# Optimization experiments

Measured on AMD Instinct MI355X. Metric: run time of the kernel, lower is better.

## Reference

```python
import jax, jax.numpy as jnp
import numpy as np
from jax import lax

BATCH = 8192
HID = 10
IN = 64
STEPS = 512
REVERSE = True


def setup_inputs() -> dict:
    key = jax.random.key(0)
    ks = jax.random.split(key, 9)
    s_in = 1.0 / np.sqrt(HID)
    return {
        "hidden": jax.random.normal(ks[0], (1, BATCH, HID), dtype=jnp.float32),
        "w_ih": jax.random.uniform(ks[1], (3 * HID, IN), jnp.float32, -s_in, s_in),
        "w_hh": jax.random.uniform(ks[2], (3 * HID, HID), jnp.float32, -s_in, s_in),
        "b_ih": jax.random.uniform(ks[3], (3 * HID,), jnp.float32, -s_in, s_in),
        "b_hh": jax.random.uniform(ks[4], (3 * HID,), jnp.float32, -s_in, s_in),
        "l1_w": jax.random.uniform(ks[5], (10, HID), jnp.float32, -s_in, s_in),
        "l1_b": jax.random.uniform(ks[6], (10,), jnp.float32, -s_in, s_in),
        "l2_w": jax.random.uniform(ks[7], (IN, 10), jnp.float32, -s_in, s_in),
        "l2_b": jax.random.uniform(ks[8], (IN,), jnp.float32, -s_in, s_in),
        "step": STEPS,
    }


def _gru_cell(h, x, w_ih, w_hh, b_ih, b_hh):
    # PyTorch GRU gate order: reset, update, new
    gi = x @ w_ih.T + b_ih  # [B, 3H]
    gh = h @ w_hh.T + b_hh  # [B, 3H]
    i_r, i_z, i_n = jnp.split(gi, 3, axis=-1)
    h_r, h_z, h_n = jnp.split(gh, 3, axis=-1)
    r = jax.nn.sigmoid(i_r + h_r)
    z = jax.nn.sigmoid(i_z + h_z)
    n = jnp.tanh(i_n + r * h_n)
    return (1.0 - z) * n + z * h


def reference(hidden, w_ih, w_hh, b_ih, b_hh, l1_w, l1_b, l2_w, l2_b, step):
    h0 = hidden[0]  # [B, H]
    B = h0.shape[0]
    x0 = jnp.zeros((B, IN), dtype=h0.dtype)  # first GRU input is zeros

    def body(carry, _):
        h, x = carry
        h_new = _gru_cell(h, x, w_ih, w_hh, b_ih, b_hh)
        o = h_new @ l1_w.T + l1_b          # l1 on GRU output
        x_next = o @ l2_w.T + l2_b         # l2 feeds next GRU step
        return (h_new, x_next), o

    _, outs = lax.scan(body, (h0, x0), None, length=step)  # [T, B, 10]
    outs = jnp.transpose(outs, (1, 0, 2))  # [B, T, 10]
    if REVERSE:
        outs = outs[:, ::-1, :]
    return outs
```

## Files before the change

kernel.cpp:

```cpp
#include <hip/hip_runtime.h>

#define HID 10
#define STEPS 512

typedef __attribute__((ext_vector_type(2))) float v2f;

template<int F>
static __device__ __forceinline__ float swz(float v) {
    return __int_as_float(__builtin_amdgcn_ds_swizzle(__float_as_int(v), (F << 5) | 0x10));
}

__global__ __launch_bounds__(64, 2) void gru_decoder_kernel(
    const float* __restrict__ hidden, const float* __restrict__ w_ih,
    const float* __restrict__ w_hh, const float* __restrict__ b_ih,
    const float* __restrict__ b_hh, const float* __restrict__ l1_w,
    const float* __restrict__ l1_b, const float* __restrict__ l2_w,
    const float* __restrict__ l2_b, float* __restrict__ out)
{
    __shared__ float sWx[640];
    __shared__ float sbx[64];
    __shared__ float sWgi[300];
    __shared__ float sbgi[30];
    __shared__ float sWhh[300];

    const int lane = threadIdx.x;
    const int f    = lane & 15;
    const int b    = blockIdx.x * 4 + (lane >> 4);
    const bool ok  = (f < HID);
    const int fi   = ok ? f : 0;

    for (int e = lane; e < 640; e += 64) {
        int i = e / 10, j = e - i * 10;
        float acc = 0.f;
        #pragma unroll
        for (int k = 0; k < 10; ++k) acc += l2_w[i * 10 + k] * l1_w[k * 10 + j];
        sWx[e] = acc;
    }
    {
        float acc = l2_b[lane];
        #pragma unroll
        for (int k = 0; k < 10; ++k) acc += l2_w[lane * 10 + k] * l1_b[k];
        sbx[lane] = acc;
    }
    for (int e = lane; e < 300; e += 64) sWhh[e] = w_hh[e];
    __syncthreads();
    for (int e = lane; e < 300; e += 64) {
        int m = e / 10, j = e - m * 10;
        float acc = 0.f;
        for (int k = 0; k < 64; ++k) acc += w_ih[m * 64 + k] * sWx[k * 10 + j];
        sWgi[e] = acc;
    }
    if (lane < 30) {
        float acc = b_ih[lane];
        for (int k = 0; k < 64; ++k) acc += w_ih[lane * 64 + k] * sbx[k];
        sbgi[lane] = acc;
    }
    __syncthreads();

    const float LOG2E = 1.4426950408889634f;
    const float S2    = 2.f * LOG2E;

    v2f wrz[10], wnn[10];
    float wo[10];
    #pragma unroll
    for (int k = 0; k < 10; ++k) {
        float grz_r = -(sWgi[fi * 10 + k] + sWhh[fi * 10 + k]) * LOG2E;
        float grz_z = -(sWgi[(10 + fi) * 10 + k] + sWhh[(10 + fi) * 10 + k]) * LOG2E;
        float gni   = sWgi[(20 + fi) * 10 + k] * S2;
        float gnh   = sWhh[(20 + fi) * 10 + k] * S2;
        wrz[k] = ok ? v2f{grz_r, grz_z} : v2f{0.f, 0.f};
        wnn[k] = ok ? v2f{gni, gnh} : v2f{0.f, 0.f};
        wo[k]  = ok ? l1_w[fi * 10 + k] : 0.f;
    }
    const v2f brz = ok ? v2f{-(sbgi[fi] + b_hh[fi]) * LOG2E,
                             -(sbgi[10 + fi] + b_hh[10 + fi]) * LOG2E}
                       : v2f{0.f, 0.f};
    const v2f bnn = ok ? v2f{sbgi[20 + fi] * S2, b_hh[20 + fi] * S2} : v2f{0.f, 0.f};
    const float bo = ok ? l1_b[fi] : 0.f;
    const v2f brz0 = ok ? v2f{-(b_ih[fi] + b_hh[fi]) * LOG2E,
                              -(b_ih[10 + fi] + b_hh[10 + fi]) * LOG2E}
                        : v2f{0.f, 0.f};
    const float bni0 = ok ? b_ih[20 + fi] * S2 : 0.f;

    float h = ok ? hidden[(size_t)b * HID + f] : 0.f;

    float ha[10];
    #define GATHER()                                                       \
        ha[0] = swz<0>(h); ha[1] = swz<1>(h); ha[2] = swz<2>(h);           \
        ha[3] = swz<3>(h); ha[4] = swz<4>(h); ha[5] = swz<5>(h);           \
        ha[6] = swz<6>(h); ha[7] = swz<7>(h); ha[8] = swz<8>(h);           \
        ha[9] = swz<9>(h);

    GATHER();

    float* pb = out + (size_t)b * (STEPS * HID) + (size_t)(STEPS - 1) * HID + f;

    #define O_AND_STORE()                                                  \
        {                                                                  \
            float o = bo;                                                  \
            _Pragma("unroll")                                              \
            for (int k = 0; k < 10; ++k) o += wo[k] * ha[k];               \
            if (ok) pb[0] = o;                                             \
            pb -= HID;                                                     \
        }

    {
        float pr = 0.f, pz = 0.f, ph = 0.f;
        #pragma unroll
        for (int k = 0; k < 10; ++k) {
            pr += sWhh[fi * 10 + k] * ha[k];
            pz += sWhh[(10 + fi) * 10 + k] * ha[k];
            ph += sWhh[(20 + fi) * 10 + k] * ha[k];
        }
        float vr = brz0.x - pr * LOG2E;
        float vz = brz0.y - pz * LOG2E;
        float r = __builtin_amdgcn_rcpf(1.f + __builtin_amdgcn_exp2f(vr));
        float z = __builtin_amdgcn_rcpf(1.f + __builtin_amdgcn_exp2f(vz));
        float y = bni0 + r * (ph * S2 + bnn.y);
        float n = 1.f - 2.f * __builtin_amdgcn_rcpf(1.f + __builtin_amdgcn_exp2f(y));
        h = ok ? (n + z * (h - n)) : 0.f;
        GATHER();
        O_AND_STORE();
    }

    #pragma unroll 1
    for (int t = 1; t < STEPS; ++t) {
        v2f arz = brz, ann = bnn;
        #pragma unroll
        for (int k = 0; k < 10; ++k) {
            v2f hh = {ha[k], ha[k]};
            arz += wrz[k] * hh;
            ann += wnn[k] * hh;
        }
        float r = __builtin_amdgcn_rcpf(1.f + __builtin_amdgcn_exp2f(arz.x));
        float z = __builtin_amdgcn_rcpf(1.f + __builtin_amdgcn_exp2f(arz.y));
        float y = ann.x + r * ann.y;
        float n = 1.f - 2.f * __builtin_amdgcn_rcpf(1.f + __builtin_amdgcn_exp2f(y));
        h = n + z * (h - n);
        GATHER();
        O_AND_STORE();
    }
}

extern "C" void kernel_launch(void* const* d_in, const int* in_sizes, int n_in,
                              void* d_out, int out_size, void* d_ws, size_t ws_size,
                              hipStream_t stream) {
    (void)in_sizes; (void)n_in; (void)d_ws; (void)ws_size; (void)out_size;
    dim3 grid(2048), block(64);
    gru_decoder_kernel<<<grid, block, 0, stream>>>(
        (const float*)d_in[0], (const float*)d_in[1], (const float*)d_in[2],
        (const float*)d_in[3], (const float*)d_in[4], (const float*)d_in[5],
        (const float*)d_in[6], (const float*)d_in[7], (const float*)d_in[8],
        (float*)d_out);
}
```

Baseline: 317.1 us.

## Replace ds_swizzle broadcasts with DPP row rotations and fuse output dot into gate loop

Replaces the ten ds_swizzle broadcasts per step with fifteen DPP row_ror rotations of h, and permutes each lane's weights so they line up with the rotated source indices. The output projection is computed from the same rotated h values inside the gate loop, with the store lagging one step and a final epilogue writing the last output. The accumulation is split into two independent chains to shorten the dependency chain. DPP moves avoid the LDS-path latency of swizzle, but the step now does 16 multiply-adds per gate instead of 10, with zero padding.

```diff
diff --git a/kernel.cpp b/kernel.cpp
--- a/kernel.cpp
+++ b/kernel.cpp
@@ -8,6 +8,16 @@
 template<int F>
 static __device__ __forceinline__ float swz(float v) {
     return __int_as_float(__builtin_amdgcn_ds_swizzle(__float_as_int(v), (F << 5) | 0x10));
+}
+
+template<int J>
+static __device__ __forceinline__ float frot(float v) {
+    return __int_as_float(__builtin_amdgcn_update_dpp(
+        0, __float_as_int(v), 0x120 + J, 0xF, 0xF, true));
+}
+template<int J>
+static __device__ __forceinline__ int irot(int v) {
+    return __builtin_amdgcn_update_dpp(0, v, 0x120 + J, 0xF, 0xF, true);
 }
 
 __global__ __launch_bounds__(64, 2) void gru_decoder_kernel(
@@ -60,18 +70,30 @@
     const float LOG2E = 1.4426950408889634f;
     const float S2    = 2.f * LOG2E;
 
-    v2f wrz[10], wnn[10];
-    float wo[10];
+    int sidx[16];
+    sidx[0]  = f;
+    sidx[1]  = irot<1>(f);   sidx[2]  = irot<2>(f);   sidx[3]  = irot<3>(f);
+    sidx[4]  = irot<4>(f);   sidx[5]  = irot<5>(f);   sidx[6]  = irot<6>(f);
+    sidx[7]  = irot<7>(f);   sidx[8]  = irot<8>(f);   sidx[9]  = irot<9>(f);
+    sidx[10] = irot<10>(f);  sidx[11] = irot<11>(f);  sidx[12] = irot<12>(f);
+    sidx[13] = irot<13>(f);  sidx[14] = irot<14>(f);  sidx[15] = irot<15>(f);
+
+    v2f wrz[16], wnn[16];
+    float wo[16];
     #pragma unroll
-    for (int k = 0; k < 10; ++k) {
-        float grz_r = -(sWgi[fi * 10 + k] + sWhh[fi * 10 + k]) * LOG2E;
-        float grz_z = -(sWgi[(10 + fi) * 10 + k] + sWhh[(10 + fi) * 10 + k]) * LOG2E;
-        float gni   = sWgi[(20 + fi) * 10 + k] * S2;
-        float gnh   = sWhh[(20 + fi) * 10 + k] * S2;
-        wrz[k] = ok ? v2f{grz_r, grz_z} : v2f{0.f, 0.f};
-        wnn[k] = ok ? v2f{gni, gnh} : v2f{0.f, 0.f};
-        wo[k]  = ok ? l1_w[fi * 10 + k] : 0.f;
-    }
+    for (int j = 0; j < 16; ++j) {
+        int s   = sidx[j];
+        bool va = ok && (s < HID);
+        int sc  = (s < HID) ? s : 0;
+        float grz_r = -(sWgi[fi * 10 + sc] + sWhh[fi * 10 + sc]) * LOG2E;
+        float grz_z = -(sWgi[(10 + fi) * 10 + sc] + sWhh[(10 + fi) * 10 + sc]) * LOG2E;
+        float gni   = sWgi[(20 + fi) * 10 + sc] * S2;
+        float gnh   = sWhh[(20 + fi) * 10 + sc] * S2;
+        wrz[j] = va ? v2f{grz_r, grz_z} : v2f{0.f, 0.f};
+        wnn[j] = va ? v2f{gni, gnh}     : v2f{0.f, 0.f};
+        wo[j]  = va ? l1_w[fi * 10 + sc] : 0.f;
+    }
+
     const v2f brz = ok ? v2f{-(sbgi[fi] + b_hh[fi]) * LOG2E,
                              -(sbgi[10 + fi] + b_hh[10 + fi]) * LOG2E}
                        : v2f{0.f, 0.f};
@@ -84,27 +106,14 @@
 
     float h = ok ? hidden[(size_t)b * HID + f] : 0.f;
 
-    float ha[10];
-    #define GATHER()                                                       \
-        ha[0] = swz<0>(h); ha[1] = swz<1>(h); ha[2] = swz<2>(h);           \
-        ha[3] = swz<3>(h); ha[4] = swz<4>(h); ha[5] = swz<5>(h);           \
-        ha[6] = swz<6>(h); ha[7] = swz<7>(h); ha[8] = swz<8>(h);           \
+    float* pb = out + (size_t)b * (STEPS * HID) + (size_t)(STEPS - 1) * HID + f;
+
+    {
+        float ha[10];
+        ha[0] = swz<0>(h); ha[1] = swz<1>(h); ha[2] = swz<2>(h);
+        ha[3] = swz<3>(h); ha[4] = swz<4>(h); ha[5] = swz<5>(h);
+        ha[6] = swz<6>(h); ha[7] = swz<7>(h); ha[8] = swz<8>(h);
         ha[9] = swz<9>(h);
-
-    GATHER();
-
-    float* pb = out + (size_t)b * (STEPS * HID) + (size_t)(STEPS - 1) * HID + f;
-
-    #define O_AND_STORE()                                                  \
-        {                                                                  \
-            float o = bo;                                                  \
-            _Pragma("unroll")                                              \
-            for (int k = 0; k < 10; ++k) o += wo[k] * ha[k];               \
-            if (ok) pb[0] = o;                                             \
-            pb -= HID;                                                     \
-        }
-
-    {
         float pr = 0.f, pz = 0.f, ph = 0.f;
         #pragma unroll
         for (int k = 0; k < 10; ++k) {
@@ -119,26 +128,65 @@
         float y = bni0 + r * (ph * S2 + bnn.y);
         float n = 1.f - 2.f * __builtin_amdgcn_rcpf(1.f + __builtin_amdgcn_exp2f(y));
         h = ok ? (n + z * (h - n)) : 0.f;
-        GATHER();
-        O_AND_STORE();
     }
 
     #pragma unroll 1
     for (int t = 1; t < STEPS; ++t) {
-        v2f arz = brz, ann = bnn;
-        #pragma unroll
-        for (int k = 0; k < 10; ++k) {
-            v2f hh = {ha[k], ha[k]};
-            arz += wrz[k] * hh;
-            ann += wnn[k] * hh;
+        float rh[16];
+        rh[0]  = h;
+        rh[1]  = frot<1>(h);   rh[2]  = frot<2>(h);   rh[3]  = frot<3>(h);
+        rh[4]  = frot<4>(h);   rh[5]  = frot<5>(h);   rh[6]  = frot<6>(h);
+        rh[7]  = frot<7>(h);   rh[8]  = frot<8>(h);   rh[9]  = frot<9>(h);
+        rh[10] = frot<10>(h);  rh[11] = frot<11>(h);  rh[12] = frot<12>(h);
+        rh[13] = frot<13>(h);  rh[14] = frot<14>(h);  rh[15] = frot<15>(h);
+
+        v2f a0 = brz, n0 = bnn;
+        v2f a1 = {0.f, 0.f}, n1 = {0.f, 0.f};
+        float o0 = bo, o1 = 0.f;
+        #pragma unroll
+        for (int j = 0; j < 8; ++j) {
+            v2f hj = {rh[j], rh[j]};
+            a0 += wrz[j] * hj;
+            n0 += wnn[j] * hj;
+            o0 = __builtin_fmaf(wo[j], rh[j], o0);
         }
+        #pragma unroll
+        for (int j = 8; j < 16; ++j) {
+            v2f hj = {rh[j], rh[j]};
+            a1 += wrz[j] * hj;
+            n1 += wnn[j] * hj;
+            o1 = __builtin_fmaf(wo[j], rh[j], o1);
+        }
+        v2f arz = a0 + a1;
+        v2f ann = n0 + n1;
+        float o = o0 + o1;
+
         float r = __builtin_amdgcn_rcpf(1.f + __builtin_amdgcn_exp2f(arz.x));
         float z = __builtin_amdgcn_rcpf(1.f + __builtin_amdgcn_exp2f(arz.y));
-        float y = ann.x + r * ann.y;
+        float zh  = z * h;
+        float omz = 1.f - z;
+        float y = __builtin_fmaf(r, ann.y, ann.x);
         float n = 1.f - 2.f * __builtin_amdgcn_rcpf(1.f + __builtin_amdgcn_exp2f(y));
-        h = n + z * (h - n);
-        GATHER();
-        O_AND_STORE();
+        h = __builtin_fmaf(n, omz, zh);
+
+        if (ok) pb[0] = o;
+        pb -= HID;
+    }
+
+    {
+        float rh[16];
+        rh[0]  = h;
+        rh[1]  = frot<1>(h);   rh[2]  = frot<2>(h);   rh[3]  = frot<3>(h);
+        rh[4]  = frot<4>(h);   rh[5]  = frot<5>(h);   rh[6]  = frot<6>(h);
+        rh[7]  = frot<7>(h);   rh[8]  = frot<8>(h);   rh[9]  = frot<9>(h);
+        rh[10] = frot<10>(h);  rh[11] = frot<11>(h);  rh[12] = frot<12>(h);
+        rh[13] = frot<13>(h);  rh[14] = frot<14>(h);  rh[15] = frot<15>(h);
+        float o0 = bo, o1 = 0.f;
+        #pragma unroll
+        for (int j = 0; j < 8; ++j)  o0 = __builtin_fmaf(wo[j], rh[j], o0);
+        #pragma unroll
+        for (int j = 8; j < 16; ++j) o1 = __builtin_fmaf(wo[j], rh[j], o1);
+        if (ok) pb[0] = o0 + o1;
     }
 }
 
```

Measured after the change: 348.5 us. +9.9%, slower.

## Fuse output projection into next step's packed matvec over h-pairs

Applied to the files above, without the earlier changes.

Repacks the weights so that packed float2 FMAs run along the reduction dimension, covering pairs of hidden elements. The output projection is folded into the same loop as the gate matvecs of the next step, with a final epilogue for the last output. This removes the separate 10-FMA output dot product from the critical path and reorders the h update so z*h can start before n is known. In exchange it adds horizontal-sum adds and a different floating-point summation order.

```diff
diff --git a/kernel.cpp b/kernel.cpp
--- a/kernel.cpp
+++ b/kernel.cpp
@@ -60,51 +60,45 @@
     const float LOG2E = 1.4426950408889634f;
     const float S2    = 2.f * LOG2E;
 
-    v2f wrz[10], wnn[10];
-    float wo[10];
+    v2f wr2[5], wz2[5], wi2[5], wh2[5], wo2[5];
     #pragma unroll
-    for (int k = 0; k < 10; ++k) {
-        float grz_r = -(sWgi[fi * 10 + k] + sWhh[fi * 10 + k]) * LOG2E;
-        float grz_z = -(sWgi[(10 + fi) * 10 + k] + sWhh[(10 + fi) * 10 + k]) * LOG2E;
-        float gni   = sWgi[(20 + fi) * 10 + k] * S2;
-        float gnh   = sWhh[(20 + fi) * 10 + k] * S2;
-        wrz[k] = ok ? v2f{grz_r, grz_z} : v2f{0.f, 0.f};
-        wnn[k] = ok ? v2f{gni, gnh} : v2f{0.f, 0.f};
-        wo[k]  = ok ? l1_w[fi * 10 + k] : 0.f;
+    for (int k2 = 0; k2 < 5; ++k2) {
+        int k0 = 2 * k2, k1 = 2 * k2 + 1;
+        float r0 = -(sWgi[fi * 10 + k0] + sWhh[fi * 10 + k0]) * LOG2E;
+        float r1 = -(sWgi[fi * 10 + k1] + sWhh[fi * 10 + k1]) * LOG2E;
+        float z0 = -(sWgi[(10 + fi) * 10 + k0] + sWhh[(10 + fi) * 10 + k0]) * LOG2E;
+        float z1 = -(sWgi[(10 + fi) * 10 + k1] + sWhh[(10 + fi) * 10 + k1]) * LOG2E;
+        float i0 = sWgi[(20 + fi) * 10 + k0] * S2;
+        float i1 = sWgi[(20 + fi) * 10 + k1] * S2;
+        float hh0 = sWhh[(20 + fi) * 10 + k0] * S2;
+        float hh1 = sWhh[(20 + fi) * 10 + k1] * S2;
+        float o0 = l1_w[fi * 10 + k0];
+        float o1 = l1_w[fi * 10 + k1];
+        wr2[k2] = ok ? v2f{r0, r1}   : v2f{0.f, 0.f};
+        wz2[k2] = ok ? v2f{z0, z1}   : v2f{0.f, 0.f};
+        wi2[k2] = ok ? v2f{i0, i1}   : v2f{0.f, 0.f};
+        wh2[k2] = ok ? v2f{hh0, hh1} : v2f{0.f, 0.f};
+        wo2[k2] = ok ? v2f{o0, o1}   : v2f{0.f, 0.f};
     }
-    const v2f brz = ok ? v2f{-(sbgi[fi] + b_hh[fi]) * LOG2E,
-                             -(sbgi[10 + fi] + b_hh[10 + fi]) * LOG2E}
-                       : v2f{0.f, 0.f};
-    const v2f bnn = ok ? v2f{sbgi[20 + fi] * S2, b_hh[20 + fi] * S2} : v2f{0.f, 0.f};
+    const float br = ok ? -(sbgi[fi] + b_hh[fi]) * LOG2E : 0.f;
+    const float bz = ok ? -(sbgi[10 + fi] + b_hh[10 + fi]) * LOG2E : 0.f;
+    const float bi = ok ? sbgi[20 + fi] * S2 : 0.f;
+    const float bh = ok ? b_hh[20 + fi] * S2 : 0.f;
     const float bo = ok ? l1_b[fi] : 0.f;
-    const v2f brz0 = ok ? v2f{-(b_ih[fi] + b_hh[fi]) * LOG2E,
-                              -(b_ih[10 + fi] + b_hh[10 + fi]) * LOG2E}
-                        : v2f{0.f, 0.f};
+    const float br0_ = ok ? -(b_ih[fi] + b_hh[fi]) * LOG2E : 0.f;
+    const float bz0_ = ok ? -(b_ih[10 + fi] + b_hh[10 + fi]) * LOG2E : 0.f;
     const float bni0 = ok ? b_ih[20 + fi] * S2 : 0.f;
 
     float h = ok ? hidden[(size_t)b * HID + f] : 0.f;
 
-    float ha[10];
-    #define GATHER()                                                       \
-        ha[0] = swz<0>(h); ha[1] = swz<1>(h); ha[2] = swz<2>(h);           \
-        ha[3] = swz<3>(h); ha[4] = swz<4>(h); ha[5] = swz<5>(h);           \
-        ha[6] = swz<6>(h); ha[7] = swz<7>(h); ha[8] = swz<8>(h);           \
-        ha[9] = swz<9>(h);
-
-    GATHER();
-
     float* pb = out + (size_t)b * (STEPS * HID) + (size_t)(STEPS - 1) * HID + f;
 
-    #define O_AND_STORE()                                                  \
-        {                                                                  \
-            float o = bo;                                                  \
-            _Pragma("unroll")                                              \
-            for (int k = 0; k < 10; ++k) o += wo[k] * ha[k];               \
-            if (ok) pb[0] = o;                                             \
-            pb -= HID;                                                     \
-        }
-
     {
+        float ha[10];
+        ha[0] = swz<0>(h); ha[1] = swz<1>(h); ha[2] = swz<2>(h);
+        ha[3] = swz<3>(h); ha[4] = swz<4>(h); ha[5] = swz<5>(h);
+        ha[6] = swz<6>(h); ha[7] = swz<7>(h); ha[8] = swz<8>(h);
+        ha[9] = swz<9>(h);
         float pr = 0.f, pz = 0.f, ph = 0.f;
         #pragma unroll
         for (int k = 0; k < 10; ++k) {
@@ -112,33 +106,64 @@
             pz += sWhh[(10 + fi) * 10 + k] * ha[k];
             ph += sWhh[(20 + fi) * 10 + k] * ha[k];
         }
-        float vr = brz0.x - pr * LOG2E;
-        float vz = brz0.y - pz * LOG2E;
+        float vr = br0_ - pr * LOG2E;
+        float vz = bz0_ - pz * LOG2E;
         float r = __builtin_amdgcn_rcpf(1.f + __builtin_amdgcn_exp2f(vr));
         float z = __builtin_amdgcn_rcpf(1.f + __builtin_amdgcn_exp2f(vz));
-        float y = bni0 + r * (ph * S2 + bnn.y);
+        float y = bni0 + r * (ph * S2 + bh);
         float n = 1.f - 2.f * __builtin_amdgcn_rcpf(1.f + __builtin_amdgcn_exp2f(y));
         h = ok ? (n + z * (h - n)) : 0.f;
-        GATHER();
-        O_AND_STORE();
     }
 
     #pragma unroll 1
     for (int t = 1; t < STEPS; ++t) {
-        v2f arz = brz, ann = bnn;
+        v2f h2[5];
+        h2[0] = v2f{swz<0>(h), swz<1>(h)};
+        h2[1] = v2f{swz<2>(h), swz<3>(h)};
+        h2[2] = v2f{swz<4>(h), swz<5>(h)};
+        h2[3] = v2f{swz<6>(h), swz<7>(h)};
+        h2[4] = v2f{swz<8>(h), swz<9>(h)};
+
+        v2f ar = {br, 0.f}, az = {bz, 0.f}, ai = {bi, 0.f},
+            ah = {bh, 0.f}, ao = {bo, 0.f};
         #pragma unroll
-        for (int k = 0; k < 10; ++k) {
-            v2f hh = {ha[k], ha[k]};
-            arz += wrz[k] * hh;
-            ann += wnn[k] * hh;
+        for (int k2 = 0; k2 < 5; ++k2) {
+            ar += wr2[k2] * h2[k2];
+            az += wz2[k2] * h2[k2];
+            ai += wi2[k2] * h2[k2];
+            ah += wh2[k2] * h2[k2];
+            ao += wo2[k2] * h2[k2];
         }
-        float r = __builtin_amdgcn_rcpf(1.f + __builtin_amdgcn_exp2f(arz.x));
-        float z = __builtin_amdgcn_rcpf(1.f + __builtin_amdgcn_exp2f(arz.y));
-        float y = ann.x + r * ann.y;
-        float n = 1.f - 2.f * __builtin_amdgcn_rcpf(1.f + __builtin_amdgcn_exp2f(y));
-        h = n + z * (h - n);
-        GATHER();
-        O_AND_STORE();
+        float arx = ar.x + ar.y;
+        float azx = az.x + az.y;
+        float aix = ai.x + ai.y;
+        float ahx = ah.x + ah.y;
+        float o   = ao.x + ao.y;
+
+        float r = __builtin_amdgcn_rcpf(1.f + __builtin_amdgcn_exp2f(arx));
+        float z = __builtin_amdgcn_rcpf(1.f + __builtin_amdgcn_exp2f(azx));
+        float zh  = z * h;
+        float omz = 1.f - z;
+        float y = __builtin_fmaf(r, ahx, aix);
+        float n = __builtin_fmaf(-2.f,
+                    __builtin_amdgcn_rcpf(1.f + __builtin_amdgcn_exp2f(y)), 1.f);
+        h = __builtin_fmaf(n, omz, zh);
+
+        if (ok) pb[0] = o;
+        pb -= HID;
+    }
+
+    {
+        v2f h2[5];
+        h2[0] = v2f{swz<0>(h), swz<1>(h)};
+        h2[1] = v2f{swz<2>(h), swz<3>(h)};
+        h2[2] = v2f{swz<4>(h), swz<5>(h)};
+        h2[3] = v2f{swz<6>(h), swz<7>(h)};
+        h2[4] = v2f{swz<8>(h), swz<9>(h)};
+        v2f ao = {bo, 0.f};
+        #pragma unroll
+        for (int k2 = 0; k2 < 5; ++k2) ao += wo2[k2] * h2[k2];
+        if (ok) pb[0] = ao.x + ao.y;
     }
 }
 
```

New measurement: 295.3 us. -6.9%, faster.

## Process two batch rows per lane with LDS broadcast and packed FMA

Applied to the files above, without the earlier changes.

Each lane now carries hidden states for two batch rows, packed into v2f so the gate and output dot products use packed-float FMAs across both rows. Hidden-state exchange moves from ten ds_swizzle ops to one LDS write plus five vector LDS reads. The GRU update is rewritten algebraically so it needs fewer reciprocals. The grid is halved and occupancy is pinned to one wave per EU, which trades latency hiding from more waves for instruction-level parallelism within each wave.

```diff
diff --git a/kernel.cpp b/kernel.cpp
--- a/kernel.cpp
+++ b/kernel.cpp
@@ -4,13 +4,15 @@
 #define STEPS 512
 
 typedef __attribute__((ext_vector_type(2))) float v2f;
+typedef __attribute__((ext_vector_type(4))) float v4f;
 
 template<int F>
 static __device__ __forceinline__ float swz(float v) {
     return __int_as_float(__builtin_amdgcn_ds_swizzle(__float_as_int(v), (F << 5) | 0x10));
 }
 
-__global__ __launch_bounds__(64, 2) void gru_decoder_kernel(
+__attribute__((amdgpu_waves_per_eu(1, 1)))
+__global__ __launch_bounds__(64) void gru_decoder_kernel(
     const float* __restrict__ hidden, const float* __restrict__ w_ih,
     const float* __restrict__ w_hh, const float* __restrict__ b_ih,
     const float* __restrict__ b_hh, const float* __restrict__ l1_w,
@@ -22,10 +24,13 @@
     __shared__ float sWgi[300];
     __shared__ float sbgi[30];
     __shared__ float sWhh[300];
+    __shared__ float sHp[144];
 
     const int lane = threadIdx.x;
     const int f    = lane & 15;
-    const int b    = blockIdx.x * 4 + (lane >> 4);
+    const int g    = lane >> 4;
+    const int bA   = blockIdx.x * 8 + g;
+    const int bB   = bA + 4;
     const bool ok  = (f < HID);
     const int fi   = ok ? f : 0;
 
@@ -60,51 +65,44 @@
     const float LOG2E = 1.4426950408889634f;
     const float S2    = 2.f * LOG2E;
 
-    v2f wrz[10], wnn[10];
-    float wo[10];
+    v2f wr2[10], wz2[10], wi2[10], wh2[10], wo2[10];
     #pragma unroll
     for (int k = 0; k < 10; ++k) {
-        float grz_r = -(sWgi[fi * 10 + k] + sWhh[fi * 10 + k]) * LOG2E;
-        float grz_z = -(sWgi[(10 + fi) * 10 + k] + sWhh[(10 + fi) * 10 + k]) * LOG2E;
-        float gni   = sWgi[(20 + fi) * 10 + k] * S2;
-        float gnh   = sWhh[(20 + fi) * 10 + k] * S2;
-        wrz[k] = ok ? v2f{grz_r, grz_z} : v2f{0.f, 0.f};
-        wnn[k] = ok ? v2f{gni, gnh} : v2f{0.f, 0.f};
-        wo[k]  = ok ? l1_w[fi * 10 + k] : 0.f;
-    }
-    const v2f brz = ok ? v2f{-(sbgi[fi] + b_hh[fi]) * LOG2E,
-                             -(sbgi[10 + fi] + b_hh[10 + fi]) * LOG2E}
-                       : v2f{0.f, 0.f};
-    const v2f bnn = ok ? v2f{sbgi[20 + fi] * S2, b_hh[20 + fi] * S2} : v2f{0.f, 0.f};
+        float rk = -(sWgi[fi * 10 + k] + sWhh[fi * 10 + k]) * LOG2E;
+        float zk = -(sWgi[(10 + fi) * 10 + k] + sWhh[(10 + fi) * 10 + k]) * LOG2E;
+        float ik = sWgi[(20 + fi) * 10 + k] * S2;
+        float hk = sWhh[(20 + fi) * 10 + k] * S2;
+        float okw = l1_w[fi * 10 + k];
+        wr2[k] = ok ? v2f{rk, rk}   : v2f{0.f, 0.f};
+        wz2[k] = ok ? v2f{zk, zk}   : v2f{0.f, 0.f};
+        wi2[k] = ok ? v2f{ik, ik}   : v2f{0.f, 0.f};
+        wh2[k] = ok ? v2f{hk, hk}   : v2f{0.f, 0.f};
+        wo2[k] = ok ? v2f{okw, okw} : v2f{0.f, 0.f};
+    }
+    const float br = ok ? -(sbgi[fi] + b_hh[fi]) * LOG2E : 0.f;
+    const float bz = ok ? -(sbgi[10 + fi] + b_hh[10 + fi]) * LOG2E : 0.f;
+    const float bi = ok ? sbgi[20 + fi] * S2 : 0.f;
+    const float bh = ok ? b_hh[20 + fi] * S2 : 0.f;
     const float bo = ok ? l1_b[fi] : 0.f;
-    const v2f brz0 = ok ? v2f{-(b_ih[fi] + b_hh[fi]) * LOG2E,
-                              -(b_ih[10 + fi] + b_hh[10 + fi]) * LOG2E}
-                        : v2f{0.f, 0.f};
+    const v2f BR2 = {br, br}, BZ2 = {bz, bz}, BI2 = {bi, bi},
+              BH2 = {bh, bh}, BO2 = {bo, bo};
+    const float br0_ = ok ? -(b_ih[fi] + b_hh[fi]) * LOG2E : 0.f;
+    const float bz0_ = ok ? -(b_ih[10 + fi] + b_hh[10 + fi]) * LOG2E : 0.f;
     const float bni0 = ok ? b_ih[20 + fi] * S2 : 0.f;
 
-    float h = ok ? hidden[(size_t)b * HID + f] : 0.f;
-
-    float ha[10];
-    #define GATHER()                                                       \
-        ha[0] = swz<0>(h); ha[1] = swz<1>(h); ha[2] = swz<2>(h);           \
-        ha[3] = swz<3>(h); ha[4] = swz<4>(h); ha[5] = swz<5>(h);           \
-        ha[6] = swz<6>(h); ha[7] = swz<7>(h); ha[8] = swz<8>(h);           \
+    float hA = ok ? hidden[(size_t)bA * HID + f] : 0.f;
+    float hB = ok ? hidden[(size_t)bB * HID + f] : 0.f;
+
+    float* pbA = out + (size_t)bA * (STEPS * HID) + (size_t)(STEPS - 1) * HID + f;
+    float* pbB = out + (size_t)bB * (STEPS * HID) + (size_t)(STEPS - 1) * HID + f;
+    float* sRow = &sHp[g * 36];
+
+    auto peel0 = [&](float& h) {
+        float ha[10];
+        ha[0] = swz<0>(h); ha[1] = swz<1>(h); ha[2] = swz<2>(h);
+        ha[3] = swz<3>(h); ha[4] = swz<4>(h); ha[5] = swz<5>(h);
+        ha[6] = swz<6>(h); ha[7] = swz<7>(h); ha[8] = swz<8>(h);
         ha[9] = swz<9>(h);
-
-    GATHER();
-
-    float* pb = out + (size_t)b * (STEPS * HID) + (size_t)(STEPS - 1) * HID + f;
-
-    #define O_AND_STORE()                                                  \
-        {                                                                  \
-            float o = bo;                                                  \
-            _Pragma("unroll")                                              \
-            for (int k = 0; k < 10; ++k) o += wo[k] * ha[k];               \
-            if (ok) pb[0] = o;                                             \
-            pb -= HID;                                                     \
-        }
-
-    {
         float pr = 0.f, pz = 0.f, ph = 0.f;
         #pragma unroll
         for (int k = 0; k < 10; ++k) {
@@ -112,33 +110,113 @@
             pz += sWhh[(10 + fi) * 10 + k] * ha[k];
             ph += sWhh[(20 + fi) * 10 + k] * ha[k];
         }
-        float vr = brz0.x - pr * LOG2E;
-        float vz = brz0.y - pz * LOG2E;
+        float vr = br0_ - pr * LOG2E;
+        float vz = bz0_ - pz * LOG2E;
         float r = __builtin_amdgcn_rcpf(1.f + __builtin_amdgcn_exp2f(vr));
         float z = __builtin_amdgcn_rcpf(1.f + __builtin_amdgcn_exp2f(vz));
-        float y = bni0 + r * (ph * S2 + bnn.y);
+        float y = bni0 + r * (ph * S2 + bh);
         float n = 1.f - 2.f * __builtin_amdgcn_rcpf(1.f + __builtin_amdgcn_exp2f(y));
         h = ok ? (n + z * (h - n)) : 0.f;
-        GATHER();
-        O_AND_STORE();
-    }
+    };
+    peel0(hA);
+    peel0(hB);
 
     #pragma unroll 1
     for (int t = 1; t < STEPS; ++t) {
-        v2f arz = brz, ann = bnn;
-        #pragma unroll
-        for (int k = 0; k < 10; ++k) {
-            v2f hh = {ha[k], ha[k]};
-            arz += wrz[k] * hh;
-            ann += wnn[k] * hh;
-        }
-        float r = __builtin_amdgcn_rcpf(1.f + __builtin_amdgcn_exp2f(arz.x));
-        float z = __builtin_amdgcn_rcpf(1.f + __builtin_amdgcn_exp2f(arz.y));
-        float y = ann.x + r * ann.y;
-        float n = 1.f - 2.f * __builtin_amdgcn_rcpf(1.f + __builtin_amdgcn_exp2f(y));
-        h = n + z * (h - n);
-        GATHER();
-        O_AND_STORE();
+        *(v2f*)(sRow + 2 * f) = v2f{hA, hB};
+        __builtin_amdgcn_wave_barrier();
+        __builtin_amdgcn_sched_barrier(0);
+        v4f q0 = *(const v4f*)(sRow);
+        v4f q1 = *(const v4f*)(sRow + 4);
+        v4f q2 = *(const v4f*)(sRow + 8);
+        v4f q3 = *(const v4f*)(sRow + 12);
+        v4f q4 = *(const v4f*)(sRow + 16);
+
+        v2f p0 = __builtin_shufflevector(q0, q0, 0, 1);
+        v2f p1 = __builtin_shufflevector(q0, q0, 2, 3);
+        v2f p2 = __builtin_shufflevector(q1, q1, 0, 1);
+        v2f p3 = __builtin_shufflevector(q1, q1, 2, 3);
+        v2f p4 = __builtin_shufflevector(q2, q2, 0, 1);
+        v2f p5 = __builtin_shufflevector(q2, q2, 2, 3);
+        v2f p6 = __builtin_shufflevector(q3, q3, 0, 1);
+        v2f p7 = __builtin_shufflevector(q3, q3, 2, 3);
+        v2f p8 = __builtin_shufflevector(q4, q4, 0, 1);
+        v2f p9 = __builtin_shufflevector(q4, q4, 2, 3);
+
+        v2f arE = wr2[0] * p0 + BR2;   v2f arO = wr2[1] * p1;
+        v2f azE = wz2[0] * p0 + BZ2;   v2f azO = wz2[1] * p1;
+        v2f aiE = wi2[0] * p0 + BI2;   v2f aiO = wi2[1] * p1;
+        v2f ahE = wh2[0] * p0 + BH2;   v2f ahO = wh2[1] * p1;
+        v2f aoE = wo2[0] * p0 + BO2;   v2f aoO = wo2[1] * p1;
+        arE += wr2[2] * p2;  arO += wr2[3] * p3;
+        azE += wz2[2] * p2;  azO += wz2[3] * p3;
+        aiE += wi2[2] * p2;  aiO += wi2[3] * p3;
+        ahE += wh2[2] * p2;  ahO += wh2[3] * p3;
+        aoE += wo2[2] * p2;  aoO += wo2[3] * p3;
+        arE += wr2[4] * p4;  arO += wr2[5] * p5;
+        azE += wz2[4] * p4;  azO += wz2[5] * p5;
+        aiE += wi2[4] * p4;  aiO += wi2[5] * p5;
+        ahE += wh2[4] * p4;  ahO += wh2[5] * p5;
+        aoE += wo2[4] * p4;  aoO += wo2[5] * p5;
+        arE += wr2[6] * p6;  arO += wr2[7] * p7;
+        azE += wz2[6] * p6;  azO += wz2[7] * p7;
+        aiE += wi2[6] * p6;  aiO += wi2[7] * p7;
+        ahE += wh2[6] * p6;  ahO += wh2[7] * p7;
+        aoE += wo2[6] * p6;  aoO += wo2[7] * p7;
+        arE += wr2[8] * p8;  arO += wr2[9] * p9;
+        azE += wz2[8] * p8;  azO += wz2[9] * p9;
+        aiE += wi2[8] * p8;  aiO += wi2[9] * p9;
+        ahE += wh2[8] * p8;  ahO += wh2[9] * p9;
+        aoE += wo2[8] * p8;  aoO += wo2[9] * p9;
+        v2f ar = arE + arO;
+        v2f az = azE + azO;
+        v2f ai = aiE + aiO;
+        v2f ah = ahE + ahO;
+        v2f ao = aoE + aoO;
+
+        float erA = __builtin_amdgcn_exp2f(ar.x);
+        float erB = __builtin_amdgcn_exp2f(ar.y);
+        float rA  = __builtin_amdgcn_rcpf(1.f + erA);
+        float rB  = __builtin_amdgcn_rcpf(1.f + erB);
+        float ezA = __builtin_amdgcn_exp2f(az.x);
+        float ezB = __builtin_amdgcn_exp2f(az.y);
+        float yA  = __builtin_fmaf(rA, ah.x, ai.x);
+        float yB  = __builtin_fmaf(rB, ah.y, ai.y);
+        float enA = __builtin_amdgcn_exp2f(yA);
+        float enB = __builtin_amdgcn_exp2f(yB);
+        float pA  = enA * ezA;             float pB  = enB * ezB;
+        float uA  = pA + (hA - ezA);       float uB  = pB + (hB - ezB);
+        float numA = __builtin_fmaf(hA, enA, uA);
+        float numB = __builtin_fmaf(hB, enB, uB);
+        float denA = (pA + (enA + ezA)) + 1.f;
+        float denB = (pB + (enB + ezB)) + 1.f;
+        hA = numA * __builtin_amdgcn_rcpf(denA);
+        hB = numB * __builtin_amdgcn_rcpf(denB);
+
+        if (ok) { pbA[0] = ao.x; pbB[0] = ao.y; }
+        pbA -= HID; pbB -= HID;
+    }
+
+    {
+        *(v2f*)(sRow + 2 * f) = v2f{hA, hB};
+        __builtin_amdgcn_wave_barrier();
+        __builtin_amdgcn_sched_barrier(0);
+        v4f q0 = *(const v4f*)(sRow);
+        v4f q1 = *(const v4f*)(sRow + 4);
+        v4f q2 = *(const v4f*)(sRow + 8);
+        v4f q3 = *(const v4f*)(sRow + 12);
+        v4f q4 = *(const v4f*)(sRow + 16);
+        v2f ao = wo2[0] * __builtin_shufflevector(q0, q0, 0, 1) + BO2;
+        ao += wo2[1] * __builtin_shufflevector(q0, q0, 2, 3);
+        ao += wo2[2] * __builtin_shufflevector(q1, q1, 0, 1);
+        ao += wo2[3] * __builtin_shufflevector(q1, q1, 2, 3);
+        ao += wo2[4] * __builtin_shufflevector(q2, q2, 0, 1);
+        ao += wo2[5] * __builtin_shufflevector(q2, q2, 2, 3);
+        ao += wo2[6] * __builtin_shufflevector(q3, q3, 0, 1);
+        ao += wo2[7] * __builtin_shufflevector(q3, q3, 2, 3);
+        ao += wo2[8] * __builtin_shufflevector(q4, q4, 0, 1);
+        ao += wo2[9] * __builtin_shufflevector(q4, q4, 2, 3);
+        if (ok) { pbA[0] = ao.x; pbB[0] = ao.y; }
     }
 }
 
@@ -146,7 +224,7 @@
                               void* d_out, int out_size, void* d_ws, size_t ws_size,
                               hipStream_t stream) {
     (void)in_sizes; (void)n_in; (void)d_ws; (void)ws_size; (void)out_size;
-    dim3 grid(2048), block(64);
+    dim3 grid(1024), block(64);
     gru_decoder_kernel<<<grid, block, 0, stream>>>(
         (const float*)d_in[0], (const float*)d_in[1], (const float*)d_in[2],
         (const float*)d_in[3], (const float*)d_in[4], (const float*)d_in[5],
```

Result: faster. 293.6 us (-7.4%).
